# Kernel optimization log

Measured on AMD Instinct MI355X. Metric: run time of the kernel, lower is better.

## Reference

```python
import jax, jax.numpy as jnp
import numpy as np
import math

D_MODEL = 1024
NUM_HEADS = 16
ALPHA, BETA, K_SCALE, C_THRESHOLD = 0.7, 0.3, 5.0, 0.3
TAU_SCHEDULE = [0.05, 0.05, 0.05, 0.15, 0.25, 0.35, 0.45, 0.55, 0.65, 0.7, 0.75, 0.8]


def setup_inputs() -> dict:
    key = jax.random.key(0)
    ks = jax.random.split(key, 6)
    B, S = 2, 1024
    scale = D_MODEL ** -0.5
    return {
        "x": jax.random.normal(ks[0], (B, S, D_MODEL), dtype=jnp.float32),
        "entropy_prev": jax.random.uniform(ks[1], (B, NUM_HEADS, S, 1), dtype=jnp.float32),
        "Wq": jax.random.normal(ks[2], (D_MODEL, D_MODEL), dtype=jnp.float32) * scale,
        "Wk": jax.random.normal(ks[3], (D_MODEL, D_MODEL), dtype=jnp.float32) * scale,
        "Wv": jax.random.normal(ks[4], (D_MODEL, D_MODEL), dtype=jnp.float32) * scale,
        "Wo": jax.random.normal(ks[5], (D_MODEL, D_MODEL), dtype=jnp.float32) * scale,
        "layer_idx": 4,
    }


def _proj(x, W, B, S, H, Dh):
    # nn.Linear(bias=False): y = x @ W.T ; then [B,S,H,Dh] -> [B,H,S,Dh]
    return jnp.einsum('bsd,ed->bse', x, W).reshape(B, S, H, Dh).transpose(0, 2, 1, 3)


def reference(x, entropy_prev, Wq, Wk, Wv, Wo, layer_idx):
    B, S, _ = x.shape
    H = NUM_HEADS
    Dh = D_MODEL // H
    tau = TAU_SCHEDULE[int(layer_idx)]

    Q = _proj(x, Wq, B, S, H, Dh)
    K = _proj(x, Wk, B, S, H, Dh)
    V = _proj(x, Wv, B, S, H, Dh)

    # raw scores [B,H,S,S]
    scores_raw = jnp.einsum('bhqd,bhkd->bhqk', Q, K) / math.sqrt(Dh)

    # key salience [B,H,1,S]
    sal = jnp.minimum((K * K).sum(axis=-1) / float(Dh), 2.0)
    sal_b = sal[:, :, None, :]

    # WIPER gate [B,H,S,S] (entropy_prev broadcasts over key dim)
    E_t = jax.nn.sigmoid(K_SCALE * (entropy_prev - C_THRESHOLD))
    gate_logit = jnp.clip(E_t * 5.0 + ALPHA * sal_b * 2.0 - BETA * entropy_prev * 1.0, -20.0, 20.0)
    gate = jax.nn.sigmoid(gate_logit)

    mask = gate >= tau
    scores_gated = jnp.where(mask, scores_raw + jnp.log(gate + 1e-8), -jnp.inf)

    best_k_idx = jnp.argmax(scores_raw, axis=-1)  # [B,H,S]
    any_finite = mask.any(axis=-1, keepdims=True)  # [B,H,S,1]

    # safe softmax: degenerate (all -inf) rows replaced by 0s, result discarded below
    attn_raw = jax.nn.softmax(jnp.where(any_finite, scores_gated, 0.0), axis=-1)
    keep_one = jax.nn.one_hot(best_k_idx, S, dtype=x.dtype)
    attn = jnp.where(any_finite, attn_raw, keep_one)

    O = jnp.einsum('bhqk,bhkd->bhqd', attn, V)

    # entropy state: S = log(l) - E[s']
    max_scores = scores_gated.max(axis=-1, keepdims=True)
    shifted = scores_gated - max_scores
    fm = jnp.isfinite(shifted)
    shifted_safe = jnp.where(fm, shifted, 0.0)
    exp_scores = jnp.where(fm, jnp.exp(shifted_safe), 0.0)
    l = jnp.maximum(exp_scores.sum(axis=-1, keepdims=True), 1e-20)
    weighted = (exp_scores * shifted_safe).sum(axis=-1, keepdims=True)
    S_state = jnp.where(any_finite, jnp.log(l) - weighted / l, 0.0)

    out = jnp.einsum('bsd,ed->bse', O.transpose(0, 2, 1, 3).reshape(B, S, D_MODEL), Wo)
    return out, S_state
```

## Files before the change

### kernel.cpp

```cpp
#include <hip/hip_runtime.h>
#include <cstdint>

#define DEVINL __device__ __forceinline__

typedef __attribute__((ext_vector_type(8))) short bf16x8;
typedef __attribute__((ext_vector_type(4))) float f32x4;
typedef __attribute__((ext_vector_type(8))) unsigned short u16x8;
typedef unsigned short u16;
typedef unsigned int u32;

#define MFMA16(a, b, c) __builtin_amdgcn_mfma_f32_16x16x32_bf16(a, b, c, 0, 0, 0)

#define LOG2E 1.4426950408889634f
#define LN2 0.69314718055994531f

DEVINL u16 f2bf(float x) {
  u32 u = __builtin_bit_cast(u32, x);
  u += 0x7FFFu + ((u >> 16) & 1u);
  return (u16)(u >> 16);
}
DEVINL float bf2f(u16 s) {
  u32 u = ((u32)s) << 16;
  return __builtin_bit_cast(float, u);
}
DEVINL float exp2fast(float x) {
  float r;
  asm("v_exp_f32 %0, %1" : "=v"(r) : "v"(x));
  return r;
}
DEVINL void gload_lds16(const void* g, void* l) {
  __builtin_amdgcn_global_load_lds(
      (const __attribute__((address_space(1))) unsigned int*)g,
      (__attribute__((address_space(3))) unsigned int*)l, 16, 0, 0);
}

__global__ __launch_bounds__(256) void k_prep(const float* __restrict__ x,
                                              const float* __restrict__ Wq,
                                              const float* __restrict__ Wk,
                                              const float* __restrict__ Wv,
                                              const float* __restrict__ Wo,
                                              const float* __restrict__ ent,
                                              u16* __restrict__ xb,
                                              u16* __restrict__ Wb,
                                              u16* __restrict__ Wob,
                                              float* __restrict__ efq) {
  const int bid = blockIdx.x;
  if (bid < 3072) {
    const float* src;
    u16* dst;
    int base;
    if (bid < 1024)      { src = x;  dst = xb;            base = bid; }
    else if (bid < 1536) { src = Wq; dst = Wb;            base = bid - 1024; }
    else if (bid < 2048) { src = Wk; dst = Wb + (1u<<20); base = bid - 1536; }
    else if (bid < 2560) { src = Wv; dst = Wb + (2u<<20); base = bid - 2048; }
    else                 { src = Wo; dst = Wob;           base = bid - 2560; }
    int i = base * 256 + threadIdx.x;
    const float4* s4 = (const float4*)src;
    float4 a = s4[2 * i], b = s4[2 * i + 1];
    u16x8 o;
    o[0] = f2bf(a.x); o[1] = f2bf(a.y); o[2] = f2bf(a.z); o[3] = f2bf(a.w);
    o[4] = f2bf(b.x); o[5] = f2bf(b.y); o[6] = f2bf(b.z); o[7] = f2bf(b.w);
    *(u16x8*)(dst + 8 * i) = o;
  } else {
    int i = (bid - 3072) * 256 + threadIdx.x;
    float e = ent[i];
    float Et = 1.f / (1.f + __expf(-5.f * (e - 0.3f)));
    efq[i] = __expf(-(5.f * Et - 0.3f * e));
  }
}

template <int BM, int BN, int NDIM, int MODE>
__global__ __launch_bounds__(256) void k_gemm(const u16* __restrict__ A,
                                              const u16* __restrict__ Bw,
                                              int Kdim, u16* __restrict__ Qo,
                                              u16* __restrict__ Ko,
                                              u16* __restrict__ Vt,
                                              float* __restrict__ egk_out,
                                              float* __restrict__ Cout) {
  constexpr int MT = BM / 32, NT = BN / 32;
  constexpr int MB = 2048 / BM, NB = NDIM / BN;
  constexpr int CPX = MB * NB / 8;
  __shared__ __align__(16) u16 SM[2][(BM + BN) * 64];
  const int t = threadIdx.x;
  const int lb = (blockIdx.x & 7) * CPX + (blockIdx.x >> 3);
  const int m0 = (lb % MB) * BM, n0 = (lb / MB) * BN;
  const int lane = t & 63, w = t >> 6;
  const int wr = w >> 1, wc = w & 1, lm = lane & 15, lg = lane >> 4;
  const int rs = t >> 3, cs = t & 7;
  f32x4 acc[MT][NT] = {};

#define GSTAGE(buf, kt)                                                        \
  {                                                                            \
    u16* As_ = SM[buf];                                                        \
    u16* Bs_ = SM[buf] + BM * 64;                                              \
    _Pragma("unroll") for (int i = 0; i < BM / 32; ++i) {                      \
      int rr = rs + 32 * i;                                                    \
      gload_lds16(A + (size_t)(m0 + rr) * Kdim + (kt) + ((cs ^ (rr & 7)) * 8), \
                  (char*)As_ + t * 16 + i * 4096);                             \
    }                                                                          \
    _Pragma("unroll") for (int i = 0; i < BN / 32; ++i) {                      \
      int rr = rs + 32 * i;                                                    \
      gload_lds16(Bw + (size_t)(n0 + rr) * Kdim + (kt) + ((cs ^ (rr & 7)) * 8),\
                  (char*)Bs_ + t * 16 + i * 4096);                             \
    }                                                                          \
  }

  GSTAGE(0, 0);
  __syncthreads();
  const int nk = Kdim >> 6;
  for (int ki = 0; ki < nk; ++ki) {
    const int cur = ki & 1;
    if (ki + 1 < nk) GSTAGE(cur ^ 1, (ki + 1) * 64);
    const u16* As = SM[cur];
    const u16* Bs = SM[cur] + BM * 64;
#pragma unroll
    for (int ks = 0; ks < 2; ++ks) {
      bf16x8 af[MT], bf[NT];
#pragma unroll
      for (int mt = 0; mt < MT; ++mt) {
        int row = wr * (BM / 2) + mt * 16 + lm;
        af[mt] = *(const bf16x8*)((const char*)As + row * 128 +
                                  (((ks * 4 + lg) ^ (row & 7)) << 4));
      }
#pragma unroll
      for (int nt = 0; nt < NT; ++nt) {
        int row = wc * (BN / 2) + nt * 16 + lm;
        bf[nt] = *(const bf16x8*)((const char*)Bs + row * 128 +
                                  (((ks * 4 + lg) ^ (row & 7)) << 4));
      }
#pragma unroll
      for (int mt = 0; mt < MT; ++mt)
#pragma unroll
        for (int nt = 0; nt < NT; ++nt)
          acc[mt][nt] = MFMA16(af[mt], bf[nt], acc[mt][nt]);
    }
    __syncthreads();
  }
#undef GSTAGE

  if (MODE == 1) {
#pragma unroll
    for (int mt = 0; mt < MT; ++mt)
#pragma unroll
      for (int nt = 0; nt < NT; ++nt)
#pragma unroll
        for (int r = 0; r < 4; ++r) {
          int m = m0 + wr * (BM / 2) + mt * 16 + lg * 4 + r;
          int n = n0 + wc * (BN / 2) + nt * 16 + lm;
          Cout[(size_t)m * 1024 + n] = acc[mt][nt][r];
        }
    return;
  }

  const int region = n0 >> 10;
  const int b = m0 >> 10, s0 = m0 & 1023;
  if (region < 2) {
    u16* dst = region == 0 ? Qo : Ko;
    const float scl = region == 0 ? 0.125f * LOG2E : 1.f;
#pragma unroll
    for (int mt = 0; mt < MT; ++mt)
#pragma unroll
      for (int nt = 0; nt < NT; ++nt)
#pragma unroll
        for (int r = 0; r < 4; ++r) {
          int m = m0 + wr * (BM / 2) + mt * 16 + lg * 4 + r;
          int n = n0 + wc * (BN / 2) + nt * 16 + lm;
          int e = n & 1023, h = e >> 6, d = e & 63;
          dst[(size_t)(((b << 4) + h) * 1024 + (m & 1023)) * 64 + d] =
              f2bf(acc[mt][nt][r] * scl);
        }
    if (region == 1) {
      int hh = ((n0 - 1024) >> 6) + wc;
#pragma unroll
      for (int mt = 0; mt < MT; ++mt)
#pragma unroll
        for (int r = 0; r < 4; ++r) {
          float ss = 0.f;
#pragma unroll
          for (int nt = 0; nt < NT; ++nt) ss += acc[mt][nt][r] * acc[mt][nt][r];
          ss += __shfl_xor(ss, 1);
          ss += __shfl_xor(ss, 2);
          ss += __shfl_xor(ss, 4);
          ss += __shfl_xor(ss, 8);
          if (lm == 0) {
            int s = s0 + wr * (BM / 2) + mt * 16 + lg * 4 + r;
            float g = 1.4f * fminf(ss * (1.f / 64.f), 2.f);
            egk_out[(size_t)(((b << 4) + hh)) * 1024 + s] = __expf(-g);
          }
        }
    }
  } else {
    u16* tile = SM[0];
#pragma unroll
    for (int half = 0; half < 2; ++half) {
      if (wc == half) {
#pragma unroll
        for (int mt = 0; mt < MT; ++mt)
#pragma unroll
          for (int nt = 0; nt < NT; ++nt)
#pragma unroll
            for (int r = 0; r < 4; ++r) {
              int d = nt * 16 + lm;
              int mloc = wr * (BM / 2) + mt * 16 + lg * 4 + r;
              tile[d * 64 + (mloc ^ ((d & 7) << 3))] = f2bf(acc[mt][nt][r]);
            }
      }
      __syncthreads();
      int hh = ((n0 - 2048) >> 6) + half;
#pragma unroll
      for (int j = 0; j < 2; ++j) {
        int dd = (t >> 3) + 32 * j, mc = t & 7;
        u16x8 v = *(const u16x8*)&tile[dd * 64 + ((mc * 8) ^ ((dd & 7) << 3))];
        *(u16x8*)(Vt + ((size_t)(((b << 4) + hh) * 64 + dd)) * 1024 + s0 + mc * 8) = v;
      }
      __syncthreads();
    }
  }
}

__global__ __launch_bounds__(256, 2) void k_attn(const u16* __restrict__ Q,
                                                 const u16* __restrict__ Kt,
                                                 const u16* __restrict__ Vt,
                                                 const float* __restrict__ efq,
                                                 const float* __restrict__ egk,
                                                 u16* __restrict__ Ob,
                                                 float* __restrict__ Sst) {
  __shared__ __align__(16) u16 Ks[2][128 * 64];
  __shared__ __align__(16) u16 Vs[2][64 * 128];
  __shared__ __align__(16) u32 Ps[4][16][64];
  const int i = blockIdx.x;
  const int lb = ((i & 7) << 6) | (i >> 3);
  const int bh = lb >> 4, qblk = lb & 15;
  const int t = threadIdx.x, lane = t & 63, w = t >> 6;
  const int lm = lane & 15, lg = lane >> 4;
  const int b = bh >> 4, h = bh & 15;
  const size_t bhS = (size_t)bh << 10;
  const int qb = qblk * 64 + w * 16;

#define STAGE(buf, k0)                                                         \
  {                                                                            \
    int rowK = t >> 3, cK = t & 7;                                             \
    int rowV = t >> 4, cV = t & 15;                                            \
    _Pragma("unroll") for (int i2 = 0; i2 < 4; ++i2) {                         \
      int rr = rowK + 32 * i2;                                                 \
      gload_lds16(Kt + (bhS + (k0) + rr) * 64 + ((cK ^ (rr & 7)) * 8),         \
                  (char*)Ks[buf] + t * 16 + i2 * 4096);                        \
      int dd2 = rowV + 16 * i2;                                                \
      gload_lds16(Vt + ((size_t)bh * 64 + dd2) * 1024 + (k0) +                 \
                      ((cV ^ (dd2 & 15)) * 8),                                 \
                  (char*)Vs[buf] + t * 16 + i2 * 4096);                        \
    }                                                                          \
  }

  bf16x8 qf[2];
#pragma unroll
  for (int ks = 0; ks < 2; ++ks)
    qf[ks] = *(const bf16x8*)(Q + (bhS + qb + lm) * 64 + ks * 32 + lg * 8);
  const float efql = efq[bhS + qb + lm];

  f32x4 Oacc[4] = {};
  float m_r = -1e30f, l_r = 0.f, W_r = 0.f;

  STAGE(0, 0);
  f32x4 egN[8];
#pragma unroll
  for (int nt = 0; nt < 8; ++nt)
    egN[nt] = *(const f32x4*)&egk[bhS + nt * 16 + lg * 4];
  __syncthreads();

  for (int kt = 0; kt < 8; ++kt) {
    const int cur = kt & 1;
    if (kt < 7) STAGE(cur ^ 1, (kt + 1) * 128);

    f32x4 c_[8];
    __builtin_amdgcn_s_setprio(1);
#pragma unroll
    for (int nt = 0; nt < 8; ++nt) {
      c_[nt] = (f32x4){0.f, 0.f, 0.f, 0.f};
#pragma unroll
      for (int ks = 0; ks < 2; ++ks) {
        int row = nt * 16 + lm;
        int byo = (((ks * 4 + lg) ^ (row & 7)) << 4);
        bf16x8 kb = *(const bf16x8*)((const char*)Ks[cur] + row * 128 + byo);
        c_[nt] = MFMA16(kb, qf[ks], c_[nt]);
      }
    }
    __builtin_amdgcn_s_setprio(0);

    float v_[8][4];
    float lmax = -3e38f;
#pragma unroll
    for (int nt = 0; nt < 8; ++nt) {
      f32x4 eg = egN[nt];
#pragma unroll
      for (int r = 0; r < 4; ++r) {
        float xg = efql * eg[r];
        v_[nt][r] = c_[nt][r] - __log2f(1.f + xg);
      }
      lmax = fmaxf(fmaxf(lmax, v_[nt][0]),
                   fmaxf(fmaxf(v_[nt][1], v_[nt][2]), v_[nt][3]));
    }
    if (kt < 7) {
#pragma unroll
      for (int nt = 0; nt < 8; ++nt)
        egN[nt] = *(const f32x4*)&egk[bhS + (kt + 1) * 128 + nt * 16 + lg * 4];
    }
    lmax = fmaxf(lmax, __shfl_xor(lmax, 16));
    lmax = fmaxf(lmax, __shfl_xor(lmax, 32));

    if (__any(lmax > m_r + 7.2134752f)) {
      float mn = fmaxf(m_r, lmax);
      float dd = m_r - mn;
      float sc = exp2fast(dd);
      W_r = sc * (W_r + dd * l_r);
      l_r *= sc;
      m_r = mn;
      float scO[4];
#pragma unroll
      for (int r = 0; r < 4; ++r) scO[r] = __shfl(sc, (lane & 48) | (lg * 4 + r));
#pragma unroll
      for (int dt = 0; dt < 4; ++dt)
#pragma unroll
        for (int r = 0; r < 4; ++r) Oacc[dt][r] *= scO[r];
    }

    float psum = 0.f, wsum = 0.f;
    u32 pw[16];
#pragma unroll
    for (int nt = 0; nt < 8; ++nt) {
      float p_[4];
#pragma unroll
      for (int r = 0; r < 4; ++r) {
        float sh = v_[nt][r] - m_r;
        float p = exp2fast(sh);
        p_[r] = p;
        psum += p;
        wsum = fmaf(p, sh, wsum);
      }
      asm("v_cvt_pk_bf16_f32 %0, %1, %2" : "=v"(pw[nt * 2 + 0]) : "v"(p_[0]), "v"(p_[1]));
      asm("v_cvt_pk_bf16_f32 %0, %1, %2" : "=v"(pw[nt * 2 + 1]) : "v"(p_[2]), "v"(p_[3]));
    }
    psum += __shfl_xor(psum, 16);
    psum += __shfl_xor(psum, 32);
    wsum += __shfl_xor(wsum, 16);
    wsum += __shfl_xor(wsum, 32);
    l_r += psum;
    W_r += wsum;

    u32* prow = &Ps[w][lm][0];
    const int sw = (lm & 7) << 2;
#pragma unroll
    for (int nt = 0; nt < 8; ++nt) {
      int idx = (nt * 8 + lg * 2) ^ sw;
      uint2 pr;
      pr.x = pw[nt * 2 + 0];
      pr.y = pw[nt * 2 + 1];
      *(uint2*)(prow + idx) = pr;
    }

    bf16x8 pa[4];
#pragma unroll
    for (int ks = 0; ks < 4; ++ks) {
      int idx = (ks * 16 + lg * 4) ^ sw;
      pa[ks] = *(const bf16x8*)(prow + idx);
    }
    __builtin_amdgcn_s_setprio(1);
#pragma unroll
    for (int dt = 0; dt < 4; ++dt) {
#pragma unroll
      for (int ks = 0; ks < 4; ++ks) {
        int row = dt * 16 + lm;
        int byo = (((ks * 4 + lg) ^ (row & 15)) << 4);
        bf16x8 vb = *(const bf16x8*)((const char*)Vs[cur] + row * 256 + byo);
        Oacc[dt] = MFMA16(pa[ks], vb, Oacc[dt]);
      }
    }
    __builtin_amdgcn_s_setprio(0);
    __syncthreads();
  }

  float invl = 1.f / l_r;
  float entv = __logf(l_r) - (W_r * LN2) * invl;
  float invO[4];
#pragma unroll
  for (int r = 0; r < 4; ++r) invO[r] = __shfl(invl, (lane & 48) | (lg * 4 + r));
#pragma unroll
  for (int dt = 0; dt < 4; ++dt)
#pragma unroll
    for (int r = 0; r < 4; ++r) {
      int srow = qb + lg * 4 + r;
      int col = h * 64 + dt * 16 + lm;
      Ob[(size_t)(b * 1024 + srow) * 1024 + col] = f2bf(Oacc[dt][r] * invO[r]);
    }
  if (lg == 0) Sst[bhS + qb + lm] = entv;
#undef STAGE
}

static constexpr size_t OFF_XB = 0;
static constexpr size_t OFF_WB = 4ull << 20;
static constexpr size_t OFF_Q = 10ull << 20;
static constexpr size_t OFF_K = 14ull << 20;
static constexpr size_t OFF_OB = 18ull << 20;
static constexpr size_t OFF_VT = 22ull << 20;
static constexpr size_t OFF_WOB = 26ull << 20;
static constexpr size_t OFF_FQ = 28ull << 20;
static constexpr size_t OFF_GK = (28ull << 20) + (128ull << 10);

extern "C" void kernel_launch(void* const* d_in, const int* in_sizes, int n_in,
                              void* d_out, int out_size, void* d_ws, size_t ws_size,
                              hipStream_t stream) {
  const float* x = (const float*)d_in[0];
  const float* ent = (const float*)d_in[1];
  const float* Wq = (const float*)d_in[2];
  const float* Wk = (const float*)d_in[3];
  const float* Wv = (const float*)d_in[4];
  const float* Wo = (const float*)d_in[5];
  (void)in_sizes; (void)n_in; (void)out_size; (void)ws_size;

  char* ws = (char*)d_ws;
  u16* xb = (u16*)(ws + OFF_XB);
  u16* Wb = (u16*)(ws + OFF_WB);
  u16* Qb = (u16*)(ws + OFF_Q);
  u16* Kb = (u16*)(ws + OFF_K);
  u16* Ob = (u16*)(ws + OFF_OB);
  u16* Vtb = (u16*)(ws + OFF_VT);
  u16* Wob = (u16*)(ws + OFF_WOB);
  float* efqd = (float*)(ws + OFF_FQ);
  float* egkd = (float*)(ws + OFF_GK);
  float* outp = (float*)d_out;
  float* Sst = outp + 2u * 1024u * 1024u;

  k_prep<<<3200, 256, 0, stream>>>(x, Wq, Wk, Wv, Wo, ent, xb, Wb, Wob, efqd);

  k_gemm<64, 128, 3072, 0><<<768, 256, 0, stream>>>(xb, Wb, 1024, Qb, Kb, Vtb,
                                                    egkd, nullptr);

  k_attn<<<512, 256, 0, stream>>>(Qb, Kb, Vtb, efqd, egkd, Ob, Sst);

  k_gemm<64, 64, 1024, 1><<<512, 256, 0, stream>>>(Ob, Wob, 1024, nullptr, nullptr,
                                                   nullptr, nullptr, outp);
}
```

Measured before the change: 67.55 us.

## Fuse all four stages into one cooperative persistent kernel with grid syncs

Merges the prep, QKV GEMM, attention and output GEMM into a single cooperative kernel of 512 blocks that separates the stages with grid.sync(). The aim is to remove three kernel-launch gaps and their tail idle time. In exchange the QKV GEMM now runs as 768 tiles over 512 blocks, which leaves an uneven second wave. Every block also uses the 80KB shared buffer and an occupancy cap of 2 blocks per CU, and each grid barrier adds its own cost. The old multi-kernel path is kept as a fallback when cooperative occupancy is too low.

```diff
diff --git a/kernel.cpp b/kernel.cpp
--- a/kernel.cpp
+++ b/kernel.cpp
@@ -1,5 +1,8 @@
 #include <hip/hip_runtime.h>
+#include <hip/hip_cooperative_groups.h>
 #include <cstdint>
+
+namespace cg = cooperative_groups;
 
 #define DEVINL __device__ __forceinline__
 
@@ -18,10 +21,6 @@
   u32 u = __builtin_bit_cast(u32, x);
   u += 0x7FFFu + ((u >> 16) & 1u);
   return (u16)(u >> 16);
-}
-DEVINL float bf2f(u16 s) {
-  u32 u = ((u32)s) << 16;
-  return __builtin_bit_cast(float, u);
 }
 DEVINL float exp2fast(float x) {
   float r;
@@ -32,6 +31,414 @@
   __builtin_amdgcn_global_load_lds(
       (const __attribute__((address_space(1))) unsigned int*)g,
       (__attribute__((address_space(3))) unsigned int*)l, 16, 0, 0);
+}
+
+static constexpr size_t OFF_XB = 0;
+static constexpr size_t OFF_WB = 4ull << 20;
+static constexpr size_t OFF_Q = 10ull << 20;
+static constexpr size_t OFF_K = 14ull << 20;
+static constexpr size_t OFF_OB = 18ull << 20;
+static constexpr size_t OFF_VT = 22ull << 20;
+static constexpr size_t OFF_WOB = 26ull << 20;
+static constexpr size_t OFF_FQ = 28ull << 20;
+static constexpr size_t OFF_GK = (28ull << 20) + (128ull << 10);
+
+__global__ __launch_bounds__(256, 2) void k_mega(
+    const float* __restrict__ x, const float* __restrict__ Wq,
+    const float* __restrict__ Wk, const float* __restrict__ Wv,
+    const float* __restrict__ Wo, const float* __restrict__ ent,
+    char* __restrict__ ws, float* __restrict__ outp) {
+  __shared__ __align__(16) char SMEM[81920];
+  u16* xb  = (u16*)(ws + OFF_XB);
+  u16* Wb  = (u16*)(ws + OFF_WB);
+  u16* Qb  = (u16*)(ws + OFF_Q);
+  u16* Kb  = (u16*)(ws + OFF_K);
+  u16* Ob  = (u16*)(ws + OFF_OB);
+  u16* Vtb = (u16*)(ws + OFF_VT);
+  u16* Wob = (u16*)(ws + OFF_WOB);
+  float* efq = (float*)(ws + OFF_FQ);
+  float* egk = (float*)(ws + OFF_GK);
+  float* Sst = outp + 2097152;
+
+  cg::grid_group grid = cg::this_grid();
+  const int bid = blockIdx.x;
+  const int t = threadIdx.x;
+  const int lane = t & 63, w = t >> 6;
+  const int lm = lane & 15, lg = lane >> 4;
+
+  {
+    const int tid = bid * 256 + t;
+    for (int g = tid; g < 786432; g += 131072) {
+      const float* src; u16* dst; int base;
+      if (g < 262144) { src = x; dst = xb; base = g; }
+      else {
+        int r = (g - 262144) >> 17;
+        base = (g - 262144) & 131071;
+        src = r == 0 ? Wq : r == 1 ? Wk : r == 2 ? Wv : Wo;
+        dst = r == 0 ? Wb : r == 1 ? Wb + 1048576 : r == 2 ? Wb + 2097152 : Wob;
+      }
+      const float4* s4 = (const float4*)src;
+      float4 a = s4[2 * base], b2 = s4[2 * base + 1];
+      u16x8 o;
+      o[0] = f2bf(a.x);  o[1] = f2bf(a.y);  o[2] = f2bf(a.z);  o[3] = f2bf(a.w);
+      o[4] = f2bf(b2.x); o[5] = f2bf(b2.y); o[6] = f2bf(b2.z); o[7] = f2bf(b2.w);
+      *(u16x8*)(dst + 8 * base) = o;
+    }
+    if (bid * 256 + t < 32768) {
+      int i = bid * 256 + t;
+      float e = ent[i];
+      float Et = 1.f / (1.f + __expf(-5.f * (e - 0.3f)));
+      efq[i] = __expf(-(5.f * Et - 0.3f * e));
+    }
+  }
+  grid.sync();
+
+  {
+    const int wr = w >> 1, wc = w & 1;
+    const int rs = t >> 3, cs = t & 7;
+    for (int tt = bid; tt < 768; tt += 512) {
+      const int m0 = (tt & 31) * 64, n0 = (tt >> 5) * 128;
+      f32x4 acc[2][4] = {};
+      auto gstage = [&](int buf, int kt) {
+        u16* As_ = (u16*)SMEM + buf * 12288;
+        u16* Bs_ = As_ + 4096;
+#pragma unroll
+        for (int i = 0; i < 2; ++i) {
+          int rr = rs + 32 * i;
+          gload_lds16(xb + (size_t)(m0 + rr) * 1024 + kt + ((cs ^ (rr & 7)) * 8),
+                      (char*)As_ + t * 16 + i * 4096);
+        }
+#pragma unroll
+        for (int i = 0; i < 4; ++i) {
+          int rr = rs + 32 * i;
+          gload_lds16(Wb + (size_t)(n0 + rr) * 1024 + kt + ((cs ^ (rr & 7)) * 8),
+                      (char*)Bs_ + t * 16 + i * 4096);
+        }
+      };
+      gstage(0, 0);
+      __syncthreads();
+      for (int ki = 0; ki < 16; ++ki) {
+        const int cur = ki & 1;
+        if (ki + 1 < 16) gstage(cur ^ 1, (ki + 1) * 64);
+        const u16* As = (u16*)SMEM + cur * 12288;
+        const u16* Bs = As + 4096;
+#pragma unroll
+        for (int ks = 0; ks < 2; ++ks) {
+          bf16x8 af[2], bfr[4];
+#pragma unroll
+          for (int mt = 0; mt < 2; ++mt) {
+            int row = wr * 32 + mt * 16 + lm;
+            af[mt] = *(const bf16x8*)((const char*)As + row * 128 +
+                                      (((ks * 4 + lg) ^ (row & 7)) << 4));
+          }
+#pragma unroll
+          for (int nt = 0; nt < 4; ++nt) {
+            int row = wc * 64 + nt * 16 + lm;
+            bfr[nt] = *(const bf16x8*)((const char*)Bs + row * 128 +
+                                       (((ks * 4 + lg) ^ (row & 7)) << 4));
+          }
+#pragma unroll
+          for (int mt = 0; mt < 2; ++mt)
+#pragma unroll
+            for (int nt = 0; nt < 4; ++nt)
+              acc[mt][nt] = MFMA16(af[mt], bfr[nt], acc[mt][nt]);
+        }
+        __syncthreads();
+      }
+      const int region = n0 >> 10;
+      const int b = m0 >> 10, s0 = m0 & 1023;
+      if (region < 2) {
+        u16* dst = region == 0 ? Qb : Kb;
+        const float scl = region == 0 ? 0.125f * LOG2E : 1.f;
+#pragma unroll
+        for (int mt = 0; mt < 2; ++mt)
+#pragma unroll
+          for (int nt = 0; nt < 4; ++nt)
+#pragma unroll
+            for (int r = 0; r < 4; ++r) {
+              int m = m0 + wr * 32 + mt * 16 + lg * 4 + r;
+              int n = n0 + wc * 64 + nt * 16 + lm;
+              int e = n & 1023, h = e >> 6, d = e & 63;
+              dst[(size_t)(((b << 4) + h) * 1024 + (m & 1023)) * 64 + d] =
+                  f2bf(acc[mt][nt][r] * scl);
+            }
+        if (region == 1) {
+          int hh = ((n0 - 1024) >> 6) + wc;
+#pragma unroll
+          for (int mt = 0; mt < 2; ++mt)
+#pragma unroll
+            for (int r = 0; r < 4; ++r) {
+              float ss = 0.f;
+#pragma unroll
+              for (int nt = 0; nt < 4; ++nt) ss += acc[mt][nt][r] * acc[mt][nt][r];
+              ss += __shfl_xor(ss, 1);
+              ss += __shfl_xor(ss, 2);
+              ss += __shfl_xor(ss, 4);
+              ss += __shfl_xor(ss, 8);
+              if (lm == 0) {
+                int s = s0 + wr * 32 + mt * 16 + lg * 4 + r;
+                float g = 1.4f * fminf(ss * (1.f / 64.f), 2.f);
+                egk[(size_t)((b << 4) + hh) * 1024 + s] = __expf(-g);
+              }
+            }
+        }
+      } else {
+        u16* tile = (u16*)SMEM;
+#pragma unroll
+        for (int half = 0; half < 2; ++half) {
+          if (wc == half) {
+#pragma unroll
+            for (int mt = 0; mt < 2; ++mt)
+#pragma unroll
+              for (int nt = 0; nt < 4; ++nt)
+#pragma unroll
+                for (int r = 0; r < 4; ++r) {
+                  int d = nt * 16 + lm;
+                  int mloc = wr * 32 + mt * 16 + lg * 4 + r;
+                  tile[d * 64 + (mloc ^ ((d & 7) << 3))] = f2bf(acc[mt][nt][r]);
+                }
+          }
+          __syncthreads();
+          int hh = ((n0 - 2048) >> 6) + half;
+#pragma unroll
+          for (int j = 0; j < 2; ++j) {
+            int dd = (t >> 3) + 32 * j, mc = t & 7;
+            u16x8 v = *(const u16x8*)&tile[dd * 64 + ((mc * 8) ^ ((dd & 7) << 3))];
+            *(u16x8*)(Vtb + ((size_t)(((b << 4) + hh) * 64 + dd)) * 1024 + s0 +
+                      mc * 8) = v;
+          }
+          __syncthreads();
+        }
+      }
+    }
+  }
+  grid.sync();
+
+  {
+    const int bh = bid >> 4, qblk = bid & 15;
+    const int b = bh >> 4, h = bh & 15;
+    const size_t bhS = (size_t)bh << 10;
+    const int qb = qblk * 64 + w * 16;
+    u16* KsA = (u16*)SMEM;
+    u16* VsA = (u16*)(SMEM + 32768);
+    u32* PsA = (u32*)(SMEM + 65536);
+
+    auto stage = [&](int buf, int k0) {
+      int rowK = t >> 3, cK = t & 7;
+      int rowV = t >> 4, cV = t & 15;
+#pragma unroll
+      for (int i2 = 0; i2 < 4; ++i2) {
+        int rr = rowK + 32 * i2;
+        gload_lds16(Kb + (bhS + k0 + rr) * 64 + ((cK ^ (rr & 7)) * 8),
+                    (char*)(KsA + buf * 8192) + t * 16 + i2 * 4096);
+        int dd2 = rowV + 16 * i2;
+        gload_lds16(Vtb + ((size_t)bh * 64 + dd2) * 1024 + k0 + ((cV ^ (dd2 & 15)) * 8),
+                    (char*)(VsA + buf * 8192) + t * 16 + i2 * 4096);
+      }
+    };
+
+    bf16x8 qf[2];
+#pragma unroll
+    for (int ks = 0; ks < 2; ++ks)
+      qf[ks] = *(const bf16x8*)(Qb + (bhS + qb + lm) * 64 + ks * 32 + lg * 8);
+    const float efql = efq[bhS + qb + lm];
+
+    f32x4 Oacc[4] = {};
+    float m_r = -1e30f, l_r = 0.f, W_r = 0.f;
+
+    stage(0, 0);
+    f32x4 egN[8];
+#pragma unroll
+    for (int nt = 0; nt < 8; ++nt)
+      egN[nt] = *(const f32x4*)&egk[bhS + nt * 16 + lg * 4];
+    __syncthreads();
+
+    for (int kt = 0; kt < 8; ++kt) {
+      const int cur = kt & 1;
+      if (kt < 7) stage(cur ^ 1, (kt + 1) * 128);
+
+      f32x4 c_[8];
+      __builtin_amdgcn_s_setprio(1);
+#pragma unroll
+      for (int nt = 0; nt < 8; ++nt) {
+        c_[nt] = (f32x4){0.f, 0.f, 0.f, 0.f};
+#pragma unroll
+        for (int ks = 0; ks < 2; ++ks) {
+          int row = nt * 16 + lm;
+          int byo = (((ks * 4 + lg) ^ (row & 7)) << 4);
+          bf16x8 kb = *(const bf16x8*)((const char*)(KsA + cur * 8192) + row * 128 + byo);
+          c_[nt] = MFMA16(kb, qf[ks], c_[nt]);
+        }
+      }
+      __builtin_amdgcn_s_setprio(0);
+
+      float v_[8][4];
+      float lmax = -3e38f;
+#pragma unroll
+      for (int nt = 0; nt < 8; ++nt) {
+        f32x4 eg = egN[nt];
+#pragma unroll
+        for (int r = 0; r < 4; ++r) {
+          float xg = efql * eg[r];
+          v_[nt][r] = c_[nt][r] - __log2f(1.f + xg);
+        }
+        lmax = fmaxf(fmaxf(lmax, v_[nt][0]),
+                     fmaxf(fmaxf(v_[nt][1], v_[nt][2]), v_[nt][3]));
+      }
+      if (kt < 7) {
+#pragma unroll
+        for (int nt = 0; nt < 8; ++nt)
+          egN[nt] = *(const f32x4*)&egk[bhS + (kt + 1) * 128 + nt * 16 + lg * 4];
+      }
+      lmax = fmaxf(lmax, __shfl_xor(lmax, 16));
+      lmax = fmaxf(lmax, __shfl_xor(lmax, 32));
+
+      if (__any(lmax > m_r + 7.2134752f)) {
+        float mn = fmaxf(m_r, lmax);
+        float dd = m_r - mn;
+        float sc = exp2fast(dd);
+        W_r = sc * (W_r + dd * l_r);
+        l_r *= sc;
+        m_r = mn;
+        float scO[4];
+#pragma unroll
+        for (int r = 0; r < 4; ++r) scO[r] = __shfl(sc, (lane & 48) | (lg * 4 + r));
+#pragma unroll
+        for (int dt = 0; dt < 4; ++dt)
+#pragma unroll
+          for (int r = 0; r < 4; ++r) Oacc[dt][r] *= scO[r];
+      }
+
+      float psum = 0.f, wsum = 0.f;
+      u32 pw[16];
+#pragma unroll
+      for (int nt = 0; nt < 8; ++nt) {
+        float p_[4];
+#pragma unroll
+        for (int r = 0; r < 4; ++r) {
+          float sh = v_[nt][r] - m_r;
+          float p = exp2fast(sh);
+          p_[r] = p;
+          psum += p;
+          wsum = fmaf(p, sh, wsum);
+        }
+        asm("v_cvt_pk_bf16_f32 %0, %1, %2" : "=v"(pw[nt*2+0]) : "v"(p_[0]), "v"(p_[1]));
+        asm("v_cvt_pk_bf16_f32 %0, %1, %2" : "=v"(pw[nt*2+1]) : "v"(p_[2]), "v"(p_[3]));
+      }
+      psum += __shfl_xor(psum, 16);
+      psum += __shfl_xor(psum, 32);
+      wsum += __shfl_xor(wsum, 16);
+      wsum += __shfl_xor(wsum, 32);
+      l_r += psum;
+      W_r += wsum;
+
+      u32* prow = PsA + (w * 16 + lm) * 64;
+      const int sw = (lm & 7) << 2;
+#pragma unroll
+      for (int nt = 0; nt < 8; ++nt) {
+        int idx = (nt * 8 + lg * 2) ^ sw;
+        uint2 pr;
+        pr.x = pw[nt * 2 + 0];
+        pr.y = pw[nt * 2 + 1];
+        *(uint2*)(prow + idx) = pr;
+      }
+
+      bf16x8 pa[4];
+#pragma unroll
+      for (int ks = 0; ks < 4; ++ks) {
+        int idx = (ks * 16 + lg * 4) ^ sw;
+        pa[ks] = *(const bf16x8*)(prow + idx);
+      }
+      __builtin_amdgcn_s_setprio(1);
+#pragma unroll
+      for (int dt = 0; dt < 4; ++dt) {
+#pragma unroll
+        for (int ks = 0; ks < 4; ++ks) {
+          int row = dt * 16 + lm;
+          int byo = (((ks * 4 + lg) ^ (row & 15)) << 4);
+          bf16x8 vb = *(const bf16x8*)((const char*)(VsA + cur * 8192) + row * 256 + byo);
+          Oacc[dt] = MFMA16(pa[ks], vb, Oacc[dt]);
+        }
+      }
+      __builtin_amdgcn_s_setprio(0);
+      __syncthreads();
+    }
+
+    float invl = 1.f / l_r;
+    float entv = __logf(l_r) - (W_r * LN2) * invl;
+    float invO[4];
+#pragma unroll
+    for (int r = 0; r < 4; ++r) invO[r] = __shfl(invl, (lane & 48) | (lg * 4 + r));
+#pragma unroll
+    for (int dt = 0; dt < 4; ++dt)
+#pragma unroll
+      for (int r = 0; r < 4; ++r) {
+        int srow = qb + lg * 4 + r;
+        int col = h * 64 + dt * 16 + lm;
+        Ob[(size_t)(b * 1024 + srow) * 1024 + col] = f2bf(Oacc[dt][r] * invO[r]);
+      }
+    if (lg == 0) Sst[bhS + qb + lm] = entv;
+  }
+  grid.sync();
+
+  {
+    const int wr = w >> 1, wc = w & 1;
+    const int rs = t >> 3, cs = t & 7;
+    const int m0 = (bid & 31) * 64, n0 = (bid >> 5) * 64;
+    f32x4 acc[2][2] = {};
+    auto gstage = [&](int buf, int kt) {
+      u16* As_ = (u16*)SMEM + buf * 8192;
+      u16* Bs_ = As_ + 4096;
+#pragma unroll
+      for (int i = 0; i < 2; ++i) {
+        int rr = rs + 32 * i;
+        gload_lds16(Ob + (size_t)(m0 + rr) * 1024 + kt + ((cs ^ (rr & 7)) * 8),
+                    (char*)As_ + t * 16 + i * 4096);
+        gload_lds16(Wob + (size_t)(n0 + rr) * 1024 + kt + ((cs ^ (rr & 7)) * 8),
+                    (char*)Bs_ + t * 16 + i * 4096);
+      }
+    };
+    gstage(0, 0);
+    __syncthreads();
+    for (int ki = 0; ki < 16; ++ki) {
+      const int cur = ki & 1;
+      if (ki + 1 < 16) gstage(cur ^ 1, (ki + 1) * 64);
+      const u16* As = (u16*)SMEM + cur * 8192;
+      const u16* Bs = As + 4096;
+#pragma unroll
+      for (int ks = 0; ks < 2; ++ks) {
+        bf16x8 af[2], bfr[2];
+#pragma unroll
+        for (int mt = 0; mt < 2; ++mt) {
+          int row = wr * 32 + mt * 16 + lm;
+          af[mt] = *(const bf16x8*)((const char*)As + row * 128 +
+                                    (((ks * 4 + lg) ^ (row & 7)) << 4));
+        }
+#pragma unroll
+        for (int nt = 0; nt < 2; ++nt) {
+          int row = wc * 32 + nt * 16 + lm;
+          bfr[nt] = *(const bf16x8*)((const char*)Bs + row * 128 +
+                                     (((ks * 4 + lg) ^ (row & 7)) << 4));
+        }
+#pragma unroll
+        for (int mt = 0; mt < 2; ++mt)
+#pragma unroll
+          for (int nt = 0; nt < 2; ++nt)
+            acc[mt][nt] = MFMA16(af[mt], bfr[nt], acc[mt][nt]);
+      }
+      __syncthreads();
+    }
+#pragma unroll
+    for (int mt = 0; mt < 2; ++mt)
+#pragma unroll
+      for (int nt = 0; nt < 2; ++nt)
+#pragma unroll
+        for (int r = 0; r < 4; ++r) {
+          int m = m0 + wr * 32 + mt * 16 + lg * 4 + r;
+          int n = n0 + wc * 32 + nt * 16 + lm;
+          outp[(size_t)m * 1024 + n] = acc[mt][nt][r];
+        }
+  }
 }
 
 __global__ __launch_bounds__(256) void k_prep(const float* __restrict__ x,
@@ -88,7 +495,6 @@
   const int wr = w >> 1, wc = w & 1, lm = lane & 15, lg = lane >> 4;
   const int rs = t >> 3, cs = t & 7;
   f32x4 acc[MT][NT] = {};
-
 #define GSTAGE(buf, kt)                                                        \
   {                                                                            \
     u16* As_ = SM[buf];                                                        \
@@ -104,7 +510,6 @@
                   (char*)Bs_ + t * 16 + i * 4096);                             \
     }                                                                          \
   }
-
   GSTAGE(0, 0);
   __syncthreads();
   const int nk = Kdim >> 6;
@@ -115,7 +520,7 @@
     const u16* Bs = SM[cur] + BM * 64;
 #pragma unroll
     for (int ks = 0; ks < 2; ++ks) {
-      bf16x8 af[MT], bf[NT];
+      bf16x8 af[MT], bfr[NT];
 #pragma unroll
       for (int mt = 0; mt < MT; ++mt) {
         int row = wr * (BM / 2) + mt * 16 + lm;
@@ -125,19 +530,18 @@
 #pragma unroll
       for (int nt = 0; nt < NT; ++nt) {
         int row = wc * (BN / 2) + nt * 16 + lm;
-        bf[nt] = *(const bf16x8*)((const char*)Bs + row * 128 +
-                                  (((ks * 4 + lg) ^ (row & 7)) << 4));
+        bfr[nt] = *(const bf16x8*)((const char*)Bs + row * 128 +
+                                   (((ks * 4 + lg) ^ (row & 7)) << 4));
       }
 #pragma unroll
       for (int mt = 0; mt < MT; ++mt)
 #pragma unroll
         for (int nt = 0; nt < NT; ++nt)
-          acc[mt][nt] = MFMA16(af[mt], bf[nt], acc[mt][nt]);
+          acc[mt][nt] = MFMA16(af[mt], bfr[nt], acc[mt][nt]);
     }
     __syncthreads();
   }
 #undef GSTAGE
-
   if (MODE == 1) {
 #pragma unroll
     for (int mt = 0; mt < MT; ++mt)
@@ -151,7 +555,6 @@
         }
     return;
   }
-
   const int region = n0 >> 10;
   const int b = m0 >> 10, s0 = m0 & 1023;
   if (region < 2) {
@@ -236,7 +639,6 @@
   const int b = bh >> 4, h = bh & 15;
   const size_t bhS = (size_t)bh << 10;
   const int qb = qblk * 64 + w * 16;
-
 #define STAGE(buf, k0)                                                         \
   {                                                                            \
     int rowK = t >> 3, cK = t & 7;                                             \
@@ -251,27 +653,22 @@
                   (char*)Vs[buf] + t * 16 + i2 * 4096);                        \
     }                                                                          \
   }
-
   bf16x8 qf[2];
 #pragma unroll
   for (int ks = 0; ks < 2; ++ks)
     qf[ks] = *(const bf16x8*)(Q + (bhS + qb + lm) * 64 + ks * 32 + lg * 8);
   const float efql = efq[bhS + qb + lm];
-
   f32x4 Oacc[4] = {};
   float m_r = -1e30f, l_r = 0.f, W_r = 0.f;
-
   STAGE(0, 0);
   f32x4 egN[8];
 #pragma unroll
   for (int nt = 0; nt < 8; ++nt)
     egN[nt] = *(const f32x4*)&egk[bhS + nt * 16 + lg * 4];
   __syncthreads();
-
   for (int kt = 0; kt < 8; ++kt) {
     const int cur = kt & 1;
     if (kt < 7) STAGE(cur ^ 1, (kt + 1) * 128);
-
     f32x4 c_[8];
     __builtin_amdgcn_s_setprio(1);
 #pragma unroll
@@ -286,7 +683,6 @@
       }
     }
     __builtin_amdgcn_s_setprio(0);
-
     float v_[8][4];
     float lmax = -3e38f;
 #pragma unroll
@@ -307,7 +703,6 @@
     }
     lmax = fmaxf(lmax, __shfl_xor(lmax, 16));
     lmax = fmaxf(lmax, __shfl_xor(lmax, 32));
-
     if (__any(lmax > m_r + 7.2134752f)) {
       float mn = fmaxf(m_r, lmax);
       float dd = m_r - mn;
@@ -323,7 +718,6 @@
 #pragma unroll
         for (int r = 0; r < 4; ++r) Oacc[dt][r] *= scO[r];
     }
-
     float psum = 0.f, wsum = 0.f;
     u32 pw[16];
 #pragma unroll
@@ -337,8 +731,8 @@
         psum += p;
         wsum = fmaf(p, sh, wsum);
       }
-      asm("v_cvt_pk_bf16_f32 %0, %1, %2" : "=v"(pw[nt * 2 + 0]) : "v"(p_[0]), "v"(p_[1]));
-      asm("v_cvt_pk_bf16_f32 %0, %1, %2" : "=v"(pw[nt * 2 + 1]) : "v"(p_[2]), "v"(p_[3]));
+      asm("v_cvt_pk_bf16_f32 %0, %1, %2" : "=v"(pw[nt*2+0]) : "v"(p_[0]), "v"(p_[1]));
+      asm("v_cvt_pk_bf16_f32 %0, %1, %2" : "=v"(pw[nt*2+1]) : "v"(p_[2]), "v"(p_[3]));
     }
     psum += __shfl_xor(psum, 16);
     psum += __shfl_xor(psum, 32);
@@ -346,7 +740,6 @@
     wsum += __shfl_xor(wsum, 32);
     l_r += psum;
     W_r += wsum;
-
     u32* prow = &Ps[w][lm][0];
     const int sw = (lm & 7) << 2;
 #pragma unroll
@@ -357,7 +750,6 @@
       pr.y = pw[nt * 2 + 1];
       *(uint2*)(prow + idx) = pr;
     }
-
     bf16x8 pa[4];
 #pragma unroll
     for (int ks = 0; ks < 4; ++ks) {
@@ -378,7 +770,6 @@
     __builtin_amdgcn_s_setprio(0);
     __syncthreads();
   }
-
   float invl = 1.f / l_r;
   float entv = __logf(l_r) - (W_r * LN2) * invl;
   float invO[4];
@@ -395,16 +786,6 @@
   if (lg == 0) Sst[bhS + qb + lm] = entv;
 #undef STAGE
 }
-
-static constexpr size_t OFF_XB = 0;
-static constexpr size_t OFF_WB = 4ull << 20;
-static constexpr size_t OFF_Q = 10ull << 20;
-static constexpr size_t OFF_K = 14ull << 20;
-static constexpr size_t OFF_OB = 18ull << 20;
-static constexpr size_t OFF_VT = 22ull << 20;
-static constexpr size_t OFF_WOB = 26ull << 20;
-static constexpr size_t OFF_FQ = 28ull << 20;
-static constexpr size_t OFF_GK = (28ull << 20) + (128ull << 10);
 
 extern "C" void kernel_launch(void* const* d_in, const int* in_sizes, int n_in,
                               void* d_out, int out_size, void* d_ws, size_t ws_size,
@@ -418,6 +799,19 @@
   (void)in_sizes; (void)n_in; (void)out_size; (void)ws_size;
 
   char* ws = (char*)d_ws;
+  float* outp = (float*)d_out;
+
+  int occ = 0;
+  hipError_t qe = hipOccupancyMaxActiveBlocksPerMultiprocessor(
+      &occ, (const void*)k_mega, 256, 0);
+  if (qe == hipSuccess && occ >= 2) {
+    void* args[8] = {(void*)&x, (void*)&Wq, (void*)&Wk, (void*)&Wv,
+                     (void*)&Wo, (void*)&ent, (void*)&ws, (void*)&outp};
+    hipLaunchCooperativeKernel((void*)k_mega, dim3(512), dim3(256), args, 0,
+                               stream);
+    return;
+  }
+
   u16* xb = (u16*)(ws + OFF_XB);
   u16* Wb = (u16*)(ws + OFF_WB);
   u16* Qb = (u16*)(ws + OFF_Q);
@@ -427,16 +821,12 @@
   u16* Wob = (u16*)(ws + OFF_WOB);
   float* efqd = (float*)(ws + OFF_FQ);
   float* egkd = (float*)(ws + OFF_GK);
-  float* outp = (float*)d_out;
   float* Sst = outp + 2u * 1024u * 1024u;
 
   k_prep<<<3200, 256, 0, stream>>>(x, Wq, Wk, Wv, Wo, ent, xb, Wb, Wob, efqd);
-
   k_gemm<64, 128, 3072, 0><<<768, 256, 0, stream>>>(xb, Wb, 1024, Qb, Kb, Vtb,
                                                     egkd, nullptr);
-
   k_attn<<<512, 256, 0, stream>>>(Qb, Kb, Vtb, efqd, egkd, Ob, Sst);
-
   k_gemm<64, 64, 1024, 1><<<512, 256, 0, stream>>>(Ob, Wob, 1024, nullptr, nullptr,
                                                    nullptr, nullptr, outp);
 }
```

After: 67.47 us. About the same (-0.1%).
